# Performance work log

Hardware: AMD Instinct MI355X
Metric: run time of the kernel (lower is better)

Reference implementation:

```python
import jax, jax.numpy as jnp
import numpy as np

B, S, D, H, DH = 4, 2048, 512, 8, 64

def setup_inputs() -> dict:
    key = jax.random.key(0)
    k1, k2, k3, k4 = jax.random.split(key, 4)
    sc = 1.0 / np.sqrt(D)
    return {
        "x": jax.random.normal(k1, (B, S, D), dtype=jnp.float32),
        "Wq": jax.random.normal(k2, (H, D, DH), dtype=jnp.float32) * sc,
        "Wk": jax.random.normal(k3, (H, D, DH), dtype=jnp.float32) * sc,
        "Wv": jax.random.normal(k4, (H, D, DH), dtype=jnp.float32) * sc,
    }

def reference(x, Wq, Wk, Wv):
    # x: [B,S,D]; Wq/Wk/Wv: [H,D,DH] (stacked per-head bias-free Linear weights)
    q = jnp.einsum('bsd,hdk->bhsk', x, Wq)
    k = jnp.einsum('bsd,hdk->bhsk', x, Wk)
    v = jnp.einsum('bsd,hdk->bhsk', x, Wv)
    scale = DH ** -0.5
    scores = jax.nn.softmax(jnp.einsum('bhqk,bhsk->bhqs', q, k) * scale, axis=-1)
    out = jnp.einsum('bhqs,bhsk->bhqk', scores, v)  # [B,H,S,DH]
    # concat heads along last dim (head order matches ModuleList order)
    return out.transpose(0, 2, 1, 3).reshape(B, S, H * DH)
```

## Files before the change

kernel.cpp:

```cpp
#include <hip/hip_runtime.h>

typedef _Float16 half8  __attribute__((ext_vector_type(8)));
typedef _Float16 half4v __attribute__((ext_vector_type(4)));
typedef _Float16 half2v __attribute__((ext_vector_type(2)));
typedef __fp16   fp16x2 __attribute__((ext_vector_type(2)));
typedef float    float4v __attribute__((ext_vector_type(4)));

__device__ __forceinline__ void async16(const _Float16* g, void* l) {
    __builtin_amdgcn_global_load_lds((const __attribute__((address_space(1))) void*)g,
                                     (__attribute__((address_space(3))) void*)l, 16, 0, 0);
}

__device__ __forceinline__ half2v pk2(float a, float b) {
    return __builtin_bit_cast(half2v, __builtin_amdgcn_cvt_pkrtz(a, b));
}
__device__ __forceinline__ half4v cat2(half2v a, half2v b) {
    return __builtin_shufflevector(a, b, 0, 1, 2, 3);
}

__global__ __launch_bounds__(256) void mha_prep(const float* __restrict__ x,
    const float* __restrict__ wq, const float* __restrict__ wk, const float* __restrict__ wv,
    _Float16* __restrict__ xh, _Float16* __restrict__ wt) {
    int t = blockIdx.x * 256 + threadIdx.x;
    const int NXH = (4 * 2048 * 512) / 4;
    if (t < NXH) {
        float4v v = ((const float4v*)x)[t];
        half4v o;
        #pragma unroll
        for (int i = 0; i < 4; ++i) o[i] = (_Float16)v[i];
        ((half4v*)xh)[t] = o;
    } else {
        int wj = t - NXH;
        int mat = wj >> 16, idx4 = wj & 65535;
        const float* w = (mat == 0) ? wq : (mat == 1) ? wk : wv;
        float4v v = ((const float4v*)w)[idx4];
        int flat = idx4 << 2;
        int h = flat >> 15, rem = flat & 32767;
        int d = rem >> 6, dh0 = rem & 63;
        _Float16* base = wt + mat * 262144 + h * 32768 + d;
        #pragma unroll
        for (int e = 0; e < 4; ++e) base[(size_t)(dh0 + e) * 512] = (_Float16)v[e];
    }
}

__global__ __launch_bounds__(256, 3) void mha_qkv(const _Float16* __restrict__ xh,
    const _Float16* __restrict__ wt, _Float16* __restrict__ Qm, _Float16* __restrict__ Km,
    _Float16* __restrict__ Vt) {
    __shared__ __align__(16) _Float16 Ash[2][128 * 32];
    __shared__ __align__(16) _Float16 Bsh[2][128 * 32];
    const int tid = threadIdx.x;
    const int lane = tid & 63, wave = tid >> 6;
    const int quad = lane >> 4, li = lane & 15;
    const int m0 = blockIdx.x * 128, n0 = blockIdx.y * 128;
    float4v acc[4][4] = {};
    const int r0 = tid >> 2, c0 = (tid & 3) ^ ((r0 >> 1) & 3);
    const int s1 = 256 + tid, r1 = s1 >> 2, c1 = (s1 & 3) ^ ((r1 >> 1) & 3);
    const _Float16* gA0 = xh + (size_t)(m0 + r0) * 512 + c0 * 8;
    const _Float16* gA1 = xh + (size_t)(m0 + r1) * 512 + c1 * 8;
    const _Float16* gB0 = wt + (size_t)(n0 + r0) * 512 + c0 * 8;
    const _Float16* gB1 = wt + (size_t)(n0 + r1) * 512 + c1 * 8;
    const int wr = (wave >> 1) * 64, wc = (wave & 1) * 64;
    const char* aB[2]; const char* bB[2];
    #pragma unroll
    for (int bb = 0; bb < 2; ++bb) {
        aB[bb] = (const char*)Ash[bb] + (wr + li) * 64 + ((quad ^ ((li >> 1) & 3)) << 4);
        bB[bb] = (const char*)Bsh[bb] + (wc + li) * 64 + ((quad ^ ((li >> 1) & 3)) << 4);
    }
    auto stage = [&](int bb, int kk) {
        async16(gA0 + kk, (char*)Ash[bb] + wave * 1024);
        async16(gA1 + kk, (char*)Ash[bb] + 4096 + wave * 1024);
        async16(gB0 + kk, (char*)Bsh[bb] + wave * 1024);
        async16(gB1 + kk, (char*)Bsh[bb] + 4096 + wave * 1024);
    };
    auto compute = [&](int bb) {
        half8 af[4], bf[4];
        #pragma unroll
        for (int mt = 0; mt < 4; ++mt) af[mt] = *(const half8*)(aB[bb] + mt * 1024);
        #pragma unroll
        for (int nt = 0; nt < 4; ++nt) bf[nt] = *(const half8*)(bB[bb] + nt * 1024);
        #pragma unroll
        for (int mt = 0; mt < 4; ++mt)
            #pragma unroll
            for (int nt = 0; nt < 4; ++nt)
                acc[mt][nt] = __builtin_amdgcn_mfma_f32_16x16x32_f16(af[mt], bf[nt], acc[mt][nt], 0, 0, 0);
    };
    stage(0, 0);
    for (int kk = 0; kk < 512; kk += 64) {
        __syncthreads();
        stage(1, kk + 32);
        compute(0);
        __syncthreads();
        if (kk + 64 < 512) stage(0, kk + 64);
        compute(1);
    }
    const int mat = n0 >> 9;
    #pragma unroll
    for (int mt = 0; mt < 4; ++mt) {
        int m = m0 + wr + mt * 16 + quad * 4;
        int b = m >> 11, s = m & 2047;
        #pragma unroll
        for (int nt = 0; nt < 4; ++nt) {
            int n = n0 + wc + nt * 16 + li;
            int h = (n >> 6) & 7, dh = n & 63;
            int bh = b * 8 + h;
            if (mat == 2) {
                half4v pkv;
                #pragma unroll
                for (int r = 0; r < 4; ++r) pkv[r] = (_Float16)acc[mt][nt][r];
                *(half4v*)(Vt + ((size_t)bh * 64 + dh) * 2048 + s) = pkv;
            } else {
                _Float16* dst = (mat == 0) ? Qm : Km;
                size_t base = ((size_t)bh * 2048 + s) * 64 + dh;
                #pragma unroll
                for (int r = 0; r < 4; ++r) dst[base + (size_t)r * 64] = (_Float16)acc[mt][nt][r];
            }
        }
    }
}

__global__ __launch_bounds__(256, 2) void mha_attn(const _Float16* __restrict__ Qm,
    const _Float16* __restrict__ Km, const _Float16* __restrict__ Vt, float* __restrict__ out) {
    __shared__ __align__(16) _Float16 KtA[2][128 * 64];
    __shared__ __align__(16) _Float16 VtA[2][64 * 128];
    const int tid = threadIdx.x, lane = tid & 63, wave = tid >> 6;
    const int quad = lane >> 4, li = lane & 15;
    const int qb = blockIdx.x, bh = blockIdx.y;
    const int b = bh >> 3, h = bh & 7;
    const _Float16* Qg = Qm + (size_t)bh * 2048 * 64;
    const _Float16* Kg = Km + (size_t)bh * 2048 * 64;
    const _Float16* Vg = Vt + (size_t)bh * 64 * 2048;
    const int q0 = qb * 128 + wave * 32;
    half8 qf[2][2];
    #pragma unroll
    for (int qt = 0; qt < 2; ++qt)
        #pragma unroll
        for (int ds = 0; ds < 2; ++ds)
            qf[qt][ds] = *(const half8*)(Qg + (size_t)(q0 + qt * 16 + li) * 64 + ds * 32 + quad * 8);
    float4v O[2][4] = {};
    float lsum[2] = {0.f, 0.f};
    const float CSC = 0.125f * 1.44269504f;
    const _Float16* pK[4]; const _Float16* pV[4];
    #pragma unroll
    for (int is = 0; is < 4; ++is) {
        int t = is * 256 + tid;
        int rk = t >> 3, ck = (t & 7) ^ (rk & 7);
        int rv = t >> 4, cv = (t & 15) ^ (rv & 15);
        pK[is] = Kg + (size_t)rk * 64 + ck * 8;
        pV[is] = Vg + (size_t)rv * 2048 + cv * 8;
    }
    auto stage = [&](int bb) {
        #pragma unroll
        for (int is = 0; is < 4; ++is) {
            async16(pK[is], (char*)KtA[bb] + is * 4096 + wave * 1024);
            async16(pV[is], (char*)VtA[bb] + is * 4096 + wave * 1024);
            pK[is] += 8192;
            pV[is] += 128;
        }
    };
    const char *kBa[2], *kBb[2], *vBq[2];
    #pragma unroll
    for (int bb = 0; bb < 2; ++bb) {
        kBa[bb] = (const char*)KtA[bb] + li * 128 + ((quad ^ (li & 7)) << 4);
        kBb[bb] = (const char*)KtA[bb] + li * 128 + (((4 + quad) ^ (li & 7)) << 4);
        vBq[bb] = (const char*)VtA[bb] + li * 256 + ((quad & 1) << 3);
    }
    auto compute = [&](int bb) {
        half2v ph[2][8][2];
        #pragma unroll
        for (int kpt = 0; kpt < 8; ++kpt) {
            half8 kf0 = *(const half8*)(kBa[bb] + kpt * 2048);
            half8 kf1 = *(const half8*)(kBb[bb] + kpt * 2048);
            float4v s0 = {}, s1 = {};
            s0 = __builtin_amdgcn_mfma_f32_16x16x32_f16(kf0, qf[0][0], s0, 0, 0, 0);
            s0 = __builtin_amdgcn_mfma_f32_16x16x32_f16(kf1, qf[0][1], s0, 0, 0, 0);
            s1 = __builtin_amdgcn_mfma_f32_16x16x32_f16(kf0, qf[1][0], s1, 0, 0, 0);
            s1 = __builtin_amdgcn_mfma_f32_16x16x32_f16(kf1, qf[1][1], s1, 0, 0, 0);
            float p0[4], p1[4];
            #pragma unroll
            for (int r = 0; r < 4; ++r) {
                p0[r] = __builtin_amdgcn_exp2f(s0[r] * CSC);
                p1[r] = __builtin_amdgcn_exp2f(s1[r] * CSC);
                lsum[0] += p0[r];
                lsum[1] += p1[r];
            }
            ph[0][kpt][0] = pk2(p0[0], p0[1]); ph[0][kpt][1] = pk2(p0[2], p0[3]);
            ph[1][kpt][0] = pk2(p1[0], p1[1]); ph[1][kpt][1] = pk2(p1[2], p1[3]);
        }
        #pragma unroll
        for (int ks = 0; ks < 8; ++ks) {
            half4v pf0 = cat2(ph[0][ks][0], ph[0][ks][1]);
            half4v pf1 = cat2(ph[1][ks][0], ph[1][ks][1]);
            int coff = (((ks * 2 + (quad >> 1)) ^ li) << 4);
            #pragma unroll
            for (int dt = 0; dt < 4; ++dt) {
                half4v vf = *(const half4v*)(vBq[bb] + dt * 4096 + coff);
                O[0][dt] = __builtin_amdgcn_mfma_f32_16x16x16f16(pf0, vf, O[0][dt], 0, 0, 0);
                O[1][dt] = __builtin_amdgcn_mfma_f32_16x16x16f16(pf1, vf, O[1][dt], 0, 0, 0);
            }
        }
    };
    stage(0);
    for (int it = 0; it < 8; ++it) {
        __syncthreads();
        stage(1);
        compute(0);
        __syncthreads();
        if (it < 7) stage(0);
        compute(1);
    }
    #pragma unroll
    for (int qt = 0; qt < 2; ++qt) {
        float l = lsum[qt];
        l += __shfl_xor(l, 16);
        l += __shfl_xor(l, 32);
        #pragma unroll
        for (int r = 0; r < 4; ++r) {
            float lr = __shfl(l, quad * 4 + r);
            float inv = 1.0f / lr;
            int q = q0 + qt * 16 + quad * 4 + r;
            float* orow = out + ((size_t)(b * 2048 + q)) * 512 + h * 64;
            #pragma unroll
            for (int dt = 0; dt < 4; ++dt) orow[dt * 16 + li] = O[qt][dt][r] * inv;
        }
    }
}

extern "C" void kernel_launch(void* const* d_in, const int* in_sizes, int n_in,
                              void* d_out, int out_size, void* d_ws, size_t ws_size,
                              hipStream_t stream) {
    const float* x  = (const float*)d_in[0];
    const float* wq = (const float*)d_in[1];
    const float* wk = (const float*)d_in[2];
    const float* wv = (const float*)d_in[3];
    float* out = (float*)d_out;
    char* ws = (char*)d_ws;
    _Float16* xh = (_Float16*)(ws);
    _Float16* wt = (_Float16*)(ws + 8388608);
    _Float16* Qm = (_Float16*)(ws + 9961472);
    _Float16* Km = (_Float16*)(ws + 18350080);
    _Float16* Vt = (_Float16*)(ws + 26738688);
    if (ws_size < 35127296u) return;
    mha_prep<<<4864, 256, 0, stream>>>(x, wq, wk, wv, xh, wt);
    mha_qkv<<<dim3(64, 12), 256, 0, stream>>>(xh, wt, Qm, Km, Vt);
    mha_attn<<<dim3(16, 32), 256, 0, stream>>>(Qm, Km, Vt, out);
}
```

Baseline: 144.4 us.

## Use 16x16x32 MFMA for PV, fold softmax scale into Q, tile weight transpose

The attention PV product moves from 16x16x16 to 16x16x32 MFMA. To make this work, K rows are loaded with a new even/odd interleaved swizzle so each lane's exponentiated scores pack directly into a half8 operand. The softmax scale times log2(e) is now applied to Q in the projection epilogue, which removes a multiply per score in the inner loop. The weight-prep kernel is split off and transposes through LDS, replacing strided scalar global writes. This adds one kernel launch, and pre-scaling Q changes fp16 rounding of Q.

```diff
diff --git a/kernel.cpp b/kernel.cpp
--- a/kernel.cpp
+++ b/kernel.cpp
@@ -6,6 +6,8 @@
 typedef __fp16   fp16x2 __attribute__((ext_vector_type(2)));
 typedef float    float4v __attribute__((ext_vector_type(4)));
 
+#define CSC 0.18033688f
+
 __device__ __forceinline__ void async16(const _Float16* g, void* l) {
     __builtin_amdgcn_global_load_lds((const __attribute__((address_space(1))) void*)g,
                                      (__attribute__((address_space(3))) void*)l, 16, 0, 0);
@@ -14,32 +16,41 @@
 __device__ __forceinline__ half2v pk2(float a, float b) {
     return __builtin_bit_cast(half2v, __builtin_amdgcn_cvt_pkrtz(a, b));
 }
-__device__ __forceinline__ half4v cat2(half2v a, half2v b) {
-    return __builtin_shufflevector(a, b, 0, 1, 2, 3);
-}
-
-__global__ __launch_bounds__(256) void mha_prep(const float* __restrict__ x,
-    const float* __restrict__ wq, const float* __restrict__ wk, const float* __restrict__ wv,
-    _Float16* __restrict__ xh, _Float16* __restrict__ wt) {
+
+__global__ __launch_bounds__(256) void mha_prep_x(const float* __restrict__ x,
+                                                  _Float16* __restrict__ xh) {
     int t = blockIdx.x * 256 + threadIdx.x;
-    const int NXH = (4 * 2048 * 512) / 4;
-    if (t < NXH) {
-        float4v v = ((const float4v*)x)[t];
-        half4v o;
-        #pragma unroll
-        for (int i = 0; i < 4; ++i) o[i] = (_Float16)v[i];
-        ((half4v*)xh)[t] = o;
-    } else {
-        int wj = t - NXH;
-        int mat = wj >> 16, idx4 = wj & 65535;
-        const float* w = (mat == 0) ? wq : (mat == 1) ? wk : wv;
-        float4v v = ((const float4v*)w)[idx4];
-        int flat = idx4 << 2;
-        int h = flat >> 15, rem = flat & 32767;
-        int d = rem >> 6, dh0 = rem & 63;
-        _Float16* base = wt + mat * 262144 + h * 32768 + d;
-        #pragma unroll
-        for (int e = 0; e < 4; ++e) base[(size_t)(dh0 + e) * 512] = (_Float16)v[e];
+    float4v v = ((const float4v*)x)[t];
+    half4v o;
+    #pragma unroll
+    for (int i = 0; i < 4; ++i) o[i] = (_Float16)v[i];
+    ((half4v*)xh)[t] = o;
+}
+
+__global__ __launch_bounds__(256) void mha_prep_w(const float* __restrict__ wq,
+    const float* __restrict__ wk, const float* __restrict__ wv, _Float16* __restrict__ wt) {
+    __shared__ __align__(16) _Float16 T[64][72];
+    const int tid = threadIdx.x;
+    const int blk = blockIdx.x;
+    const int dt = blk & 7, h = (blk >> 3) & 7, mat = blk >> 6;
+    const float* w = ((mat == 0) ? wq : (mat == 1) ? wk : wv) + h * 32768 + dt * 64 * 64;
+    #pragma unroll
+    for (int i = 0; i < 4; ++i) {
+        int s = tid + i * 256;
+        int dl = s >> 4, c4 = s & 15;
+        float4v v = ((const float4v*)(w + (size_t)dl * 64))[c4];
+        #pragma unroll
+        for (int e = 0; e < 4; ++e) T[c4 * 4 + e][dl] = (_Float16)v[e];
+    }
+    __syncthreads();
+    #pragma unroll
+    for (int i = 0; i < 2; ++i) {
+        int s = tid + i * 256;
+        int dh = s >> 3, c8 = s & 7;
+        half8 o;
+        #pragma unroll
+        for (int e = 0; e < 8; ++e) o[e] = T[dh][c8 * 8 + e];
+        *(half8*)(wt + (size_t)((mat * 8 + h) * 64 + dh) * 512 + dt * 64 + c8 * 8) = o;
     }
 }
 
@@ -94,6 +105,7 @@
         compute(1);
     }
     const int mat = n0 >> 9;
+    const float osc = (mat == 0) ? CSC : 1.0f;
     #pragma unroll
     for (int mt = 0; mt < 4; ++mt) {
         int m = m0 + wr + mt * 16 + quad * 4;
@@ -112,7 +124,7 @@
                 _Float16* dst = (mat == 0) ? Qm : Km;
                 size_t base = ((size_t)bh * 2048 + s) * 64 + dh;
                 #pragma unroll
-                for (int r = 0; r < 4; ++r) dst[base + (size_t)r * 64] = (_Float16)acc[mt][nt][r];
+                for (int r = 0; r < 4; ++r) dst[base + (size_t)r * 64] = (_Float16)(acc[mt][nt][r] * osc);
             }
         }
     }
@@ -138,14 +150,14 @@
             qf[qt][ds] = *(const half8*)(Qg + (size_t)(q0 + qt * 16 + li) * 64 + ds * 32 + quad * 8);
     float4v O[2][4] = {};
     float lsum[2] = {0.f, 0.f};
-    const float CSC = 0.125f * 1.44269504f;
     const _Float16* pK[4]; const _Float16* pV[4];
     #pragma unroll
     for (int is = 0; is < 4; ++is) {
-        int t = is * 256 + tid;
-        int rk = t >> 3, ck = (t & 7) ^ (rk & 7);
-        int rv = t >> 4, cv = (t & 15) ^ (rv & 15);
-        pK[is] = Kg + (size_t)rk * 64 + ck * 8;
+        int s = is * 256 + tid;
+        int rk = s >> 3, sck = s & 7;
+        int swk = (rk & 3) | (((rk >> 3) & 1) << 2);
+        int rv = s >> 4, cv = (s & 15) ^ (rv & 15);
+        pK[is] = Kg + (size_t)rk * 64 + (sck ^ swk) * 8;
         pV[is] = Vg + (size_t)rv * 2048 + cv * 8;
     }
     auto stage = [&](int bb) {
@@ -157,45 +169,54 @@
             pV[is] += 128;
         }
     };
-    const char *kBa[2], *kBb[2], *vBq[2];
+    const int rowE = ((li >> 2) << 3) | (li & 3);
+    const int swzE = (li & 3) | (((li >> 2) & 1) << 2);
+    const char *k0e[2], *k1e[2], *vBq[2];
     #pragma unroll
     for (int bb = 0; bb < 2; ++bb) {
-        kBa[bb] = (const char*)KtA[bb] + li * 128 + ((quad ^ (li & 7)) << 4);
-        kBb[bb] = (const char*)KtA[bb] + li * 128 + (((4 + quad) ^ (li & 7)) << 4);
-        vBq[bb] = (const char*)VtA[bb] + li * 256 + ((quad & 1) << 3);
-    }
+        const char* base = (const char*)KtA[bb] + rowE * 128;
+        k0e[bb] = base + ((quad ^ swzE) << 4);
+        k1e[bb] = base + (((quad + 4) ^ swzE) << 4);
+        vBq[bb] = (const char*)VtA[bb] + li * 256;
+    }
+    int coff[4];
+    #pragma unroll
+    for (int c = 0; c < 4; ++c) coff[c] = ((c * 4 + quad) ^ li) << 4;
     auto compute = [&](int bb) {
-        half2v ph[2][8][2];
-        #pragma unroll
-        for (int kpt = 0; kpt < 8; ++kpt) {
-            half8 kf0 = *(const half8*)(kBa[bb] + kpt * 2048);
-            half8 kf1 = *(const half8*)(kBb[bb] + kpt * 2048);
-            float4v s0 = {}, s1 = {};
-            s0 = __builtin_amdgcn_mfma_f32_16x16x32_f16(kf0, qf[0][0], s0, 0, 0, 0);
-            s0 = __builtin_amdgcn_mfma_f32_16x16x32_f16(kf1, qf[0][1], s0, 0, 0, 0);
-            s1 = __builtin_amdgcn_mfma_f32_16x16x32_f16(kf0, qf[1][0], s1, 0, 0, 0);
-            s1 = __builtin_amdgcn_mfma_f32_16x16x32_f16(kf1, qf[1][1], s1, 0, 0, 0);
-            float p0[4], p1[4];
-            #pragma unroll
-            for (int r = 0; r < 4; ++r) {
-                p0[r] = __builtin_amdgcn_exp2f(s0[r] * CSC);
-                p1[r] = __builtin_amdgcn_exp2f(s1[r] * CSC);
-                lsum[0] += p0[r];
-                lsum[1] += p1[r];
+        #pragma unroll
+        for (int c = 0; c < 4; ++c) {
+            half8 f0e = *(const half8*)(k0e[bb] + c * 4096);
+            half8 f1e = *(const half8*)(k1e[bb] + c * 4096);
+            half8 f0o = *(const half8*)(k0e[bb] + c * 4096 + 512);
+            half8 f1o = *(const half8*)(k1e[bb] + c * 4096 + 512);
+            float4v se[2] = {}, so[2] = {};
+            se[0] = __builtin_amdgcn_mfma_f32_16x16x32_f16(f0e, qf[0][0], se[0], 0, 0, 0);
+            se[0] = __builtin_amdgcn_mfma_f32_16x16x32_f16(f1e, qf[0][1], se[0], 0, 0, 0);
+            se[1] = __builtin_amdgcn_mfma_f32_16x16x32_f16(f0e, qf[1][0], se[1], 0, 0, 0);
+            se[1] = __builtin_amdgcn_mfma_f32_16x16x32_f16(f1e, qf[1][1], se[1], 0, 0, 0);
+            so[0] = __builtin_amdgcn_mfma_f32_16x16x32_f16(f0o, qf[0][0], so[0], 0, 0, 0);
+            so[0] = __builtin_amdgcn_mfma_f32_16x16x32_f16(f1o, qf[0][1], so[0], 0, 0, 0);
+            so[1] = __builtin_amdgcn_mfma_f32_16x16x32_f16(f0o, qf[1][0], so[1], 0, 0, 0);
+            so[1] = __builtin_amdgcn_mfma_f32_16x16x32_f16(f1o, qf[1][1], so[1], 0, 0, 0);
+            half8 pf[2];
+            #pragma unroll
+            for (int qt = 0; qt < 2; ++qt) {
+                float pe[4], po[4];
+                #pragma unroll
+                for (int r = 0; r < 4; ++r) {
+                    pe[r] = __builtin_amdgcn_exp2f(se[qt][r]);
+                    po[r] = __builtin_amdgcn_exp2f(so[qt][r]);
+                    lsum[qt] += pe[r] + po[r];
+                }
+                half4v a = __builtin_shufflevector(pk2(pe[0], pe[1]), pk2(pe[2], pe[3]), 0, 1, 2, 3);
+                half4v o = __builtin_shufflevector(pk2(po[0], po[1]), pk2(po[2], po[3]), 0, 1, 2, 3);
+                pf[qt] = __builtin_shufflevector(a, o, 0, 1, 2, 3, 4, 5, 6, 7);
             }
-            ph[0][kpt][0] = pk2(p0[0], p0[1]); ph[0][kpt][1] = pk2(p0[2], p0[3]);
-            ph[1][kpt][0] = pk2(p1[0], p1[1]); ph[1][kpt][1] = pk2(p1[2], p1[3]);
-        }
-        #pragma unroll
-        for (int ks = 0; ks < 8; ++ks) {
-            half4v pf0 = cat2(ph[0][ks][0], ph[0][ks][1]);
-            half4v pf1 = cat2(ph[1][ks][0], ph[1][ks][1]);
-            int coff = (((ks * 2 + (quad >> 1)) ^ li) << 4);
             #pragma unroll
             for (int dt = 0; dt < 4; ++dt) {
-                half4v vf = *(const half4v*)(vBq[bb] + dt * 4096 + coff);
-                O[0][dt] = __builtin_amdgcn_mfma_f32_16x16x16f16(pf0, vf, O[0][dt], 0, 0, 0);
-                O[1][dt] = __builtin_amdgcn_mfma_f32_16x16x16f16(pf1, vf, O[1][dt], 0, 0, 0);
+                half8 vf = *(const half8*)(vBq[bb] + dt * 4096 + coff[c]);
+                O[0][dt] = __builtin_amdgcn_mfma_f32_16x16x32_f16(pf[0], vf, O[0][dt], 0, 0, 0);
+                O[1][dt] = __builtin_amdgcn_mfma_f32_16x16x32_f16(pf[1], vf, O[1][dt], 0, 0, 0);
             }
         }
     };
@@ -240,7 +261,8 @@
     _Float16* Km = (_Float16*)(ws + 18350080);
     _Float16* Vt = (_Float16*)(ws + 26738688);
     if (ws_size < 35127296u) return;
-    mha_prep<<<4864, 256, 0, stream>>>(x, wq, wk, wv, xh, wt);
+    mha_prep_x<<<4096, 256, 0, stream>>>(x, xh);
+    mha_prep_w<<<192, 256, 0, stream>>>(wq, wk, wv, wt);
     mha_qkv<<<dim3(64, 12), 256, 0, stream>>>(xh, wt, Qm, Km, Vt);
     mha_attn<<<dim3(16, 32), 256, 0, stream>>>(Qm, Km, Vt, out);
 }
```

Result: faster. 138.4 us (-4.2%).
